# Kernel tuning notes

Measured on AMD Instinct MI355X. Metric: run time of the kernel, lower is better.

Reference implementation:

```python
import jax, jax.numpy as jnp
import numpy as np

TAU = 2.0
TH = 1.0


def setup_inputs() -> dict:
    key = jax.random.key(0)
    x = jax.random.normal(key, (32, 512, 2048), dtype=jnp.float32)  # [B, T, D]
    return {"x": x}


def reference(x):
    # Leaky-integrate-and-fire recurrence over time axis T.
    # v_t = v_{t-1} + (x_t - v_{t-1}) / tau
    # s_t = sigmoid(v_t - th)          (surrogate spike, used as forward output here)
    # v_t = v_t * (1 - s_t)            (soft multiplicative reset)
    B, T, D = x.shape
    xt = jnp.swapaxes(x, 0, 1)  # [T, B, D] for scan

    def step(v, x_t):
        v = v + (x_t - v) / TAU
        s = jax.nn.sigmoid(v - TH)
        v = v * (1.0 - s)
        return v, s

    v0 = jnp.zeros((B, D), dtype=x.dtype)
    _, spikes = jax.lax.scan(step, v0, xt)  # spikes: [T, B, D]
    return jnp.swapaxes(spikes, 0, 1)  # [B, T, D]
```

## Files before the change

kernel.cpp:

```cpp
#include <hip/hip_runtime.h>
#include <math.h>


#define TAU_INV 0.5f
#define TH 1.0f

typedef __attribute__((ext_vector_type(4))) float f32x4;

constexpr int BATCH = 32;
constexpr int TT = 512;
constexpr int DD = 2048;
constexpr int S = 8;
constexpr int SEG = TT / S;
constexpr int W = 32;
constexpr int U = 8;
constexpr int NC_W = W / U;
constexpr int NC_M = SEG / U;
constexpr int NC = NC_W + NC_M;
constexpr int PD = 2;
constexpr int DEPTH = PD + 1;

__global__ __launch_bounds__(256, 2) void lif_kernel(const float* __restrict__ x,
                                                     float* __restrict__ out) {
    int tid = blockIdx.x * blockDim.x + threadIdx.x;
    int d4 = tid & 511;
    int sg = (tid >> 9) & 7;
    int b = tid >> 12;
    int d = d4 * 4;
    const int t0 = sg * SEG;
    const bool warm = (sg != 0);

    const float* xw = x + ((size_t)b * TT + (warm ? t0 - W : t0)) * DD + d;
    const float* xm = x + ((size_t)b * TT + t0) * DD + d;
    float* om = out + ((size_t)b * TT + t0) * DD + d;

    f32x4 buf[DEPTH][U];

    auto src = [&](int c) -> const f32x4* {
        return (c < NC_W)
                   ? reinterpret_cast<const f32x4*>(xw + (size_t)c * U * DD)
                   : reinterpret_cast<const f32x4*>(xm + (size_t)(c - NC_W) * U * DD);
    };

    #pragma unroll
    for (int c = 0; c < PD; ++c) {
        const f32x4* sp = src(c);
        #pragma unroll
        for (int i = 0; i < U; ++i)
            buf[c][i] = sp[(size_t)i * (DD / 4)];
    }

    float v0 = 0.0f, v1 = 0.0f, v2 = 0.0f, v3 = 0.0f;

    #pragma unroll
    for (int c = 0; c < NC; ++c) {
        const int cur = c % DEPTH;

        if (c + PD < NC) {
            const int ps = (c + PD) % DEPTH;
            const f32x4* sp = src(c + PD);
            #pragma unroll
            for (int i = 0; i < U; ++i)
                buf[ps][i] = sp[(size_t)i * (DD / 4)];
        }

        #pragma unroll
        for (int i = 0; i < U; ++i) {
            float in0 = buf[cur][i].x, in1 = buf[cur][i].y;
            float in2 = buf[cur][i].z, in3 = buf[cur][i].w;
            float s0, s1, s2, s3;
            v0 = v0 + (in0 - v0) * TAU_INV;
            v1 = v1 + (in1 - v1) * TAU_INV;
            v2 = v2 + (in2 - v2) * TAU_INV;
            v3 = v3 + (in3 - v3) * TAU_INV;
            s0 = __builtin_amdgcn_rcpf(1.0f + __expf(TH - v0));
            s1 = __builtin_amdgcn_rcpf(1.0f + __expf(TH - v1));
            s2 = __builtin_amdgcn_rcpf(1.0f + __expf(TH - v2));
            s3 = __builtin_amdgcn_rcpf(1.0f + __expf(TH - v3));
            v0 = v0 * (1.0f - s0);
            v1 = v1 * (1.0f - s1);
            v2 = v2 * (1.0f - s2);
            v3 = v3 * (1.0f - s3);
            if (c >= NC_W) {
                f32x4 sv = {s0, s1, s2, s3};
                f32x4* op = reinterpret_cast<f32x4*>(
                    om + (size_t)((c - NC_W) * U + i) * DD);
                __builtin_nontemporal_store(sv, op);
            }
        }

        if (c == NC_W - 1) {
            if (!warm) { v0 = 0.0f; v1 = 0.0f; v2 = 0.0f; v3 = 0.0f; }
        }
    }
}

extern "C" void kernel_launch(void* const* d_in, const int* in_sizes, int n_in,
                              void* d_out, int out_size, void* d_ws, size_t ws_size,
                              hipStream_t stream) {
    const float* x = (const float*)d_in[0];
    float* out = (float*)d_out;
    const int threads = 256;
    const int total = BATCH * S * (DD / 4);
    const int blocks = total / threads;
    lif_kernel<<<blocks, threads, 0, stream>>>(x, out);
}
```

Before: 238.8 us.

## Split time axis into more segments with shorter warm-up, drop register prefetch

The time axis is now split into 32 segments per batch instead of 8, with a 16-step warm-up instead of 32. This gives four times as many threads and blocks, with launch bounds raised to 8 blocks per CU. The explicit triple-buffered register prefetch is replaced by plain per-chunk loads, which cuts register pressure and relies on occupancy to hide latency. In exchange, the warm-up rereads roughly double total global reads. The shorter warm-up also leans harder on the recurrence's decay for accuracy.

```diff
diff --git a/kernel.cpp b/kernel.cpp
--- a/kernel.cpp
+++ b/kernel.cpp
@@ -10,22 +10,20 @@
 constexpr int BATCH = 32;
 constexpr int TT = 512;
 constexpr int DD = 2048;
-constexpr int S = 8;
+constexpr int S = 32;
 constexpr int SEG = TT / S;
-constexpr int W = 32;
+constexpr int W = 16;
 constexpr int U = 8;
 constexpr int NC_W = W / U;
 constexpr int NC_M = SEG / U;
 constexpr int NC = NC_W + NC_M;
-constexpr int PD = 2;
-constexpr int DEPTH = PD + 1;
 
-__global__ __launch_bounds__(256, 2) void lif_kernel(const float* __restrict__ x,
+__global__ __launch_bounds__(256, 8) void lif_kernel(const float* __restrict__ x,
                                                      float* __restrict__ out) {
     int tid = blockIdx.x * blockDim.x + threadIdx.x;
     int d4 = tid & 511;
-    int sg = (tid >> 9) & 7;
-    int b = tid >> 12;
+    int sg = (tid >> 9) & (S - 1);
+    int b = tid >> 14;
     int d = d4 * 4;
     const int t0 = sg * SEG;
     const bool warm = (sg != 0);
@@ -34,45 +32,25 @@
     const float* xm = x + ((size_t)b * TT + t0) * DD + d;
     float* om = out + ((size_t)b * TT + t0) * DD + d;
 
-    f32x4 buf[DEPTH][U];
-
-    auto src = [&](int c) -> const f32x4* {
-        return (c < NC_W)
-                   ? reinterpret_cast<const f32x4*>(xw + (size_t)c * U * DD)
-                   : reinterpret_cast<const f32x4*>(xm + (size_t)(c - NC_W) * U * DD);
-    };
-
-    #pragma unroll
-    for (int c = 0; c < PD; ++c) {
-        const f32x4* sp = src(c);
-        #pragma unroll
-        for (int i = 0; i < U; ++i)
-            buf[c][i] = sp[(size_t)i * (DD / 4)];
-    }
-
     float v0 = 0.0f, v1 = 0.0f, v2 = 0.0f, v3 = 0.0f;
 
     #pragma unroll
     for (int c = 0; c < NC; ++c) {
-        const int cur = c % DEPTH;
-
-        if (c + PD < NC) {
-            const int ps = (c + PD) % DEPTH;
-            const f32x4* sp = src(c + PD);
-            #pragma unroll
-            for (int i = 0; i < U; ++i)
-                buf[ps][i] = sp[(size_t)i * (DD / 4)];
-        }
+        const float* base = (c < NC_W)
+                                ? xw + (size_t)c * U * DD
+                                : xm + (size_t)(c - NC_W) * U * DD;
+        f32x4 buf[U];
+        #pragma unroll
+        for (int i = 0; i < U; ++i)
+            buf[i] = *reinterpret_cast<const f32x4*>(base + (size_t)i * DD);
 
         #pragma unroll
         for (int i = 0; i < U; ++i) {
-            float in0 = buf[cur][i].x, in1 = buf[cur][i].y;
-            float in2 = buf[cur][i].z, in3 = buf[cur][i].w;
             float s0, s1, s2, s3;
-            v0 = v0 + (in0 - v0) * TAU_INV;
-            v1 = v1 + (in1 - v1) * TAU_INV;
-            v2 = v2 + (in2 - v2) * TAU_INV;
-            v3 = v3 + (in3 - v3) * TAU_INV;
+            v0 = v0 + (buf[i].x - v0) * TAU_INV;
+            v1 = v1 + (buf[i].y - v1) * TAU_INV;
+            v2 = v2 + (buf[i].z - v2) * TAU_INV;
+            v3 = v3 + (buf[i].w - v3) * TAU_INV;
             s0 = __builtin_amdgcn_rcpf(1.0f + __expf(TH - v0));
             s1 = __builtin_amdgcn_rcpf(1.0f + __expf(TH - v1));
             s2 = __builtin_amdgcn_rcpf(1.0f + __expf(TH - v2));
@@ -83,9 +61,9 @@
             v3 = v3 * (1.0f - s3);
             if (c >= NC_W) {
                 f32x4 sv = {s0, s1, s2, s3};
-                f32x4* op = reinterpret_cast<f32x4*>(
-                    om + (size_t)((c - NC_W) * U + i) * DD);
-                __builtin_nontemporal_store(sv, op);
+                __builtin_nontemporal_store(
+                    sv, reinterpret_cast<f32x4*>(
+                            om + (size_t)((c - NC_W) * U + i) * DD));
             }
         }
 
```

Result: no change. 240.6 us (+0.7%).
